# Kernel optimization log

Measured on AMD Instinct MI355X. Metric: run time of the kernel, lower is better.

The kernel has to match this reference:

```python
import jax, jax.numpy as jnp
import numpy as np

Y_SCALE = 1.0   # from init_kwargs
EPS = 1e-12     # matches torch F.normalize eps


def _l2_normalize(x):
    n = jnp.linalg.norm(x, axis=-1, keepdims=True)
    return x / jnp.maximum(n, EPS)


def _sequence_similarity(a, b):
    # a: [B, N, D], b: [B, M, D]
    a = _l2_normalize(a)
    b = _l2_normalize(b)
    cos_sims = jnp.einsum('bnd,bmd->bnm', a, b)  # [B, N, M]
    if cos_sims.shape[-1] > cos_sims.shape[-2]:
        max_sims = cos_sims.max(axis=-1)  # [B, N]
    else:
        max_sims = cos_sims.max(axis=-2)  # [B, M]
    return max_sims.mean(axis=-1)  # [B]


def setup_inputs() -> dict:
    key = jax.random.key(0)
    k1, k2, k3 = jax.random.split(key, 3)
    B, N, M, D = 16, 4096, 2048, 256
    x1 = jax.random.normal(k1, (B, N, D), dtype=jnp.float32)
    x2 = jax.random.normal(k2, (B, M, D), dtype=jnp.float32)
    y = jax.random.uniform(k3, (B,), dtype=jnp.float32)
    return {"x1": x1, "x2": x2, "y": y}


def reference(x1, x2, y):
    raw_sim_scores = _sequence_similarity(x1, x2)  # [B]
    losses = (raw_sim_scores - y) ** 2
    scales = jnp.where(y != 0.0, jnp.float32(Y_SCALE), jnp.float32(1.0))
    return (losses * scales).sum()
```

## Files before the change

### kernel.cpp

```cpp
#include <hip/hip_runtime.h>
#include <hip/hip_bf16.h>
#include <cstdint>
#include <cstddef>

#define BATCH 16
#define NROWS 4096
#define MROWS 2048
#define DDIM  256
#define NSPLIT 2
#define NCHUNKS 8

typedef __attribute__((ext_vector_type(8)))  int   i32x8;
typedef __attribute__((ext_vector_type(16))) float f32x16;

__global__ void __launch_bounds__(256) norm_cast(
    const float* __restrict__ x1, const float* __restrict__ x2,
    unsigned char* __restrict__ aout, unsigned char* __restrict__ bout) {
  const int wid  = threadIdx.x >> 6;
  const int lane = threadIdx.x & 63;
  const long long row = (long long)blockIdx.x * 4 + wid;
  const long long R1 = (long long)BATCH * NROWS;
  const long long R2 = (long long)BATCH * MROWS;
  if (row >= R1 + R2) return;
  const float* src; unsigned char* dst;
  if (row < R1) { src = x1 + row * DDIM; dst = aout + row * DDIM; }
  else { long long r2 = row - R1; src = x2 + r2 * DDIM; dst = bout + r2 * DDIM; }
  float4 v = ((const float4*)src)[lane];
  float ss = v.x*v.x + v.y*v.y + v.z*v.z + v.w*v.w;
  #pragma unroll
  for (int o = 32; o >= 1; o >>= 1) ss += __shfl_xor(ss, o, 64);
  float sc = 1.0f / fmaxf(sqrtf(ss), 1e-12f);
  int r = __builtin_amdgcn_cvt_pk_fp8_f32(v.x * sc, v.y * sc, 0, false);
  r = __builtin_amdgcn_cvt_pk_fp8_f32(v.z * sc, v.w * sc, r, true);
  ((unsigned int*)dst)[lane] = (unsigned int)r;
}

typedef __attribute__((address_space(1))) const void gas_t;
typedef __attribute__((address_space(3))) void las_t;
#define GLL16(g, l) __builtin_amdgcn_global_load_lds((gas_t*)(g), (las_t*)(l), 16, 0, 0)

#define LDSA(S) (lds + ((S) << 14))
#define LDSB(S) (lds + 65536 + ((S) << 14))

static __device__ __forceinline__ i32x8 frag8(const char* slot, int row, int lane) {
  const int rb = (lane >> 1) & 3;
  const int ks = lane >> 5;
  const char* base = slot + row * 64;
  uint4 u0 = *(const uint4*)(base + ((((ks << 1) | 0) ^ rb) << 4));
  uint4 u1 = *(const uint4*)(base + ((((ks << 1) | 1) ^ rb) << 4));
  i32x8 r;
  r[0] = u0.x; r[1] = u0.y; r[2] = u0.z; r[3] = u0.w;
  r[4] = u1.x; r[5] = u1.y; r[6] = u1.z; r[7] = u1.w;
  return r;
}

__global__ void __launch_bounds__(512, 1) maxsim_fp8(
    const unsigned char* __restrict__ A,
    const unsigned char* __restrict__ Bm,
    float* __restrict__ partials)
{
  __shared__ __align__(16) char lds[131072];

  const int t = threadIdx.x;
  const int lane = t & 63;
  const int w = t >> 6;
  const int wr = w >> 2;
  const int wc = w & 3;
  const int l31 = lane & 31;

  const int hw = blockIdx.x;
  const int logical = (hw & 7) * 32 + (hw >> 3);
  const int mt = logical & 7;
  const int grp = logical >> 3;
  const int sp = grp & 1;
  const int bb = grp >> 1;

  const int m0 = mt * 256;
  const int nbase = sp * (NROWS / NSPLIT);

  const unsigned char* Aba = A  + (size_t)bb * NROWS * DDIM;
  const unsigned char* Bba = Bm + ((size_t)bb * MROWS + m0) * DDIM;

  const int r0 = (w * 2 + 0) * 16 + (lane >> 2);
  const int r1 = (w * 2 + 1) * 16 + (lane >> 2);
  const int sph = (((lane & 3) ^ ((lane >> 3) & 3)) << 4);
  const unsigned char* sA0 = Aba + (size_t)r0 * DDIM + sph;
  const unsigned char* sA1 = Aba + (size_t)r1 * DDIM + sph;
  const unsigned char* sB0 = Bba + (size_t)r0 * DDIM + sph;
  const unsigned char* sB1 = Bba + (size_t)r1 * DDIM + sph;
  const int l0 = (w * 2 + 0) * 1024 + lane * 16;
  const int l1 = (w * 2 + 1) * 1024 + lane * 16;

  #define STAGE_A(SLOT, OFF) do { \
    GLL16(sA0 + (OFF), (SLOT) + l0); GLL16(sA1 + (OFF), (SLOT) + l1); } while (0)
  #define STAGE_B(SLOT, OFF) do { \
    GLL16(sB0 + (OFF), (SLOT) + l0); GLL16(sB1 + (OFF), (SLOT) + l1); } while (0)

  f32x16 acc[4][2] = {};
  const f32x16 z16 = {};
  i32x8 af[4];
  i32x8 bfAll[4][2];
  float cm[2] = {-INFINITY, -INFINITY};

  STAGE_A(LDSA(0), (size_t)nbase * DDIM + 0);
  STAGE_B(LDSB(0), 0);
  STAGE_B(LDSB(1), 64);
  STAGE_B(LDSB(2), 128);
  STAGE_B(LDSB(3), 192);
  STAGE_A(LDSA(1), (size_t)nbase * DDIM + 64);
  asm volatile("s_waitcnt vmcnt(2)" ::: "memory");
  asm volatile("s_barrier" ::: "memory");

  #pragma unroll
  for (int kt = 0; kt < 4; ++kt)
    #pragma unroll
    for (int nj = 0; nj < 2; ++nj)
      bfAll[kt][nj] = frag8(LDSB(kt), wc * 64 + nj * 32 + l31, lane);

  for (int nc = 0; nc < NCHUNKS; ++nc) {
    #pragma unroll
    for (int kt = 0; kt < 4; ++kt) {
      const char* sa = LDSA(kt);
      const int s2 = (kt + 2) & 3;
      const int nc2 = (kt < 2) ? nc : ((nc + 1) & (NCHUNKS - 1));
      const size_t offA2 = ((size_t)nbase + nc2 * 256) * DDIM + s2 * 64;

      #pragma unroll
      for (int mi = 0; mi < 4; ++mi)
        af[mi] = frag8(sa, wr * 128 + mi * 32 + l31, lane);
      STAGE_A(LDSA(s2), offA2);
      #pragma unroll
      for (int mi = 0; mi < 4; ++mi)
        #pragma unroll
        for (int nj = 0; nj < 2; ++nj)
          acc[mi][nj] = __builtin_amdgcn_mfma_scale_f32_32x32x64_f8f6f4(
              af[mi], bfAll[kt][nj], acc[mi][nj], 0, 0,
              0, 0x7F7F7F7F, 0, 0x7F7F7F7F);
      asm volatile("s_waitcnt vmcnt(2)" ::: "memory");
      asm volatile("s_barrier" ::: "memory");
    }
    #pragma unroll
    for (int nj = 0; nj < 2; ++nj) {
      float v = cm[nj];
      #pragma unroll
      for (int mi = 0; mi < 4; ++mi) {
        #pragma unroll
        for (int r = 0; r < 16; ++r) v = fmaxf(v, acc[mi][nj][r]);
        acc[mi][nj] = z16;
      }
      cm[nj] = v;
    }
  }

  asm volatile("s_waitcnt vmcnt(0)" ::: "memory");
  asm volatile("s_barrier" ::: "memory");
  #pragma unroll
  for (int nj = 0; nj < 2; ++nj)
    cm[nj] = fmaxf(cm[nj], __shfl_xor(cm[nj], 32, 64));
  float* cmax = (float*)lds;
  if (lane < 32) {
    cmax[wr * 256 + wc * 64 + l31]      = cm[0];
    cmax[wr * 256 + wc * 64 + 32 + l31] = cm[1];
  }
  __syncthreads();
  if (t < 256) {
    float v = fmaxf(cmax[t], cmax[256 + t]);
    partials[((size_t)sp * BATCH + bb) * MROWS + m0 + t] = v;
  }
}

__global__ void __launch_bounds__(256) batch_loss(
    const float* __restrict__ partials, const float* __restrict__ y,
    float* __restrict__ bloss) {
  __shared__ float red[4];
  const int b = blockIdx.x;
  const int t = threadIdx.x;
  const int lane = t & 63;
  const int w = t >> 6;
  float s = 0.0f;
  for (int m = t; m < MROWS; m += 256) {
    float v = partials[(size_t)b * MROWS + m];
    #pragma unroll
    for (int sp = 1; sp < NSPLIT; ++sp)
      v = fmaxf(v, partials[((size_t)sp * BATCH + b) * MROWS + m]);
    s += v;
  }
  #pragma unroll
  for (int o = 32; o >= 1; o >>= 1) s += __shfl_xor(s, o, 64);
  if (lane == 0) red[w] = s;
  __syncthreads();
  if (t == 0) {
    float sum = red[0] + red[1] + red[2] + red[3];
    float mean = sum / (float)MROWS;
    float yb = y[b];
    float d = mean - yb;
    bloss[b] = d * d;
  }
}

__global__ void __launch_bounds__(64) final_sum(
    const float* __restrict__ bloss, float* __restrict__ out) {
  const int t = threadIdx.x;
  float v = (t < BATCH) ? bloss[t] : 0.0f;
  #pragma unroll
  for (int o = 32; o >= 1; o >>= 1) v += __shfl_xor(v, o, 64);
  if (t == 0) out[0] = v;
}

extern "C" void kernel_launch(void* const* d_in, const int* in_sizes, int n_in,
                              void* d_out, int out_size, void* d_ws, size_t ws_size,
                              hipStream_t stream) {
  const float* x1 = (const float*)d_in[0];
  const float* x2 = (const float*)d_in[1];
  const float* y  = (const float*)d_in[2];
  float* out = (float*)d_out;

  unsigned char* aF8 = (unsigned char*)d_ws;
  unsigned char* bF8 = aF8 + (size_t)BATCH * NROWS * DDIM;
  float* partials = (float*)(bF8 + (size_t)BATCH * MROWS * DDIM);
  float* bloss = partials + (size_t)NSPLIT * BATCH * MROWS;

  const int totRows = BATCH * (NROWS + MROWS);
  norm_cast<<<(totRows + 3) / 4, 256, 0, stream>>>(x1, x2, aF8, bF8);
  maxsim_fp8<<<BATCH * 8 * NSPLIT, 512, 0, stream>>>(aF8, bF8, partials);
  batch_loss<<<BATCH, 256, 0, stream>>>(partials, y, bloss);
  final_sum<<<1, 64, 0, stream>>>(bloss, out);
}
```

Before: 54.82 us.

## Deepen A-tile prefetch ring to eight LDS slots and halve barrier count

```diff
diff --git a/kernel.cpp b/kernel.cpp
--- a/kernel.cpp
+++ b/kernel.cpp
@@ -39,8 +39,7 @@
 typedef __attribute__((address_space(3))) void las_t;
 #define GLL16(g, l) __builtin_amdgcn_global_load_lds((gas_t*)(g), (las_t*)(l), 16, 0, 0)
 
-#define LDSA(S) (lds + ((S) << 14))
-#define LDSB(S) (lds + 65536 + ((S) << 14))
+#define SLOT(S) (lds + ((S) << 14))
 
 static __device__ __forceinline__ i32x8 frag8(const char* slot, int row, int lane) {
   const int rb = (lane >> 1) & 3;
@@ -91,10 +90,12 @@
   const int l0 = (w * 2 + 0) * 1024 + lane * 16;
   const int l1 = (w * 2 + 1) * 1024 + lane * 16;
 
-  #define STAGE_A(SLOT, OFF) do { \
-    GLL16(sA0 + (OFF), (SLOT) + l0); GLL16(sA1 + (OFF), (SLOT) + l1); } while (0)
-  #define STAGE_B(SLOT, OFF) do { \
-    GLL16(sB0 + (OFF), (SLOT) + l0); GLL16(sB1 + (OFF), (SLOT) + l1); } while (0)
+  #define STAGE_A(SL, OFF) do { \
+    GLL16(sA0 + (OFF), (SL) + l0); GLL16(sA1 + (OFF), (SL) + l1); } while (0)
+  #define STAGE_B(SL, OFF) do { \
+    GLL16(sB0 + (OFF), (SL) + l0); GLL16(sB1 + (OFF), (SL) + l1); } while (0)
+
+  #define AOFF(G) (((size_t)nbase + (((G) >> 2) & 7) * 256) * DDIM + ((G) & 3) * 64)
 
   f32x16 acc[4][2] = {};
   const f32x16 z16 = {};
@@ -102,53 +103,78 @@
   i32x8 bfAll[4][2];
   float cm[2] = {-INFINITY, -INFINITY};
 
-  STAGE_A(LDSA(0), (size_t)nbase * DDIM + 0);
-  STAGE_B(LDSB(0), 0);
-  STAGE_B(LDSB(1), 64);
-  STAGE_B(LDSB(2), 128);
-  STAGE_B(LDSB(3), 192);
-  STAGE_A(LDSA(1), (size_t)nbase * DDIM + 64);
-  asm volatile("s_waitcnt vmcnt(2)" ::: "memory");
+  STAGE_A(SLOT(0), AOFF(0));
+  STAGE_B(SLOT(4), 0);
+  STAGE_B(SLOT(5), 64);
+  STAGE_B(SLOT(6), 128);
+  STAGE_B(SLOT(7), 192);
+  STAGE_A(SLOT(1), AOFF(1));
+  STAGE_A(SLOT(2), AOFF(2));
+  STAGE_A(SLOT(3), AOFF(3));
+  asm volatile("s_waitcnt vmcnt(0)" ::: "memory");
   asm volatile("s_barrier" ::: "memory");
 
   #pragma unroll
   for (int kt = 0; kt < 4; ++kt)
     #pragma unroll
     for (int nj = 0; nj < 2; ++nj)
-      bfAll[kt][nj] = frag8(LDSB(kt), wc * 64 + nj * 32 + l31, lane);
-
-  for (int nc = 0; nc < NCHUNKS; ++nc) {
+      bfAll[kt][nj] = frag8(SLOT(4 + kt), wc * 64 + nj * 32 + l31, lane);
+  asm volatile("s_waitcnt lgkmcnt(0)" ::: "memory");
+  asm volatile("s_barrier" ::: "memory");
+  STAGE_A(SLOT(4), AOFF(4));
+  STAGE_A(SLOT(5), AOFF(5));
+
+  for (int jj = 0; jj < 4; ++jj) {
     #pragma unroll
-    for (int kt = 0; kt < 4; ++kt) {
-      const char* sa = LDSA(kt);
-      const int s2 = (kt + 2) & 3;
-      const int nc2 = (kt < 2) ? nc : ((nc + 1) & (NCHUNKS - 1));
-      const size_t offA2 = ((size_t)nbase + nc2 * 256) * DDIM + s2 * 64;
-
-      #pragma unroll
-      for (int mi = 0; mi < 4; ++mi)
-        af[mi] = frag8(sa, wr * 128 + mi * 32 + l31, lane);
-      STAGE_A(LDSA(s2), offA2);
+    for (int p = 0; p < 4; ++p) {
+      const int J = jj * 4 + p;
+      const int sa0 = 2 * p;
+      const int sa1 = 2 * p + 1;
+      const int st0 = (2 * p + 6) & 7;
+      const int st1 = (2 * p + 7) & 7;
+      const int kt0 = (2 * p) & 3;
+      const int kt1 = (2 * p + 1) & 3;
+      const int g0 = (2 * J + 6) & 31;
+      const int g1 = (2 * J + 7) & 31;
+
+      #pragma unroll
+      for (int mi = 0; mi < 4; ++mi)
+        af[mi] = frag8(SLOT(sa0), wr * 128 + mi * 32 + l31, lane);
+      STAGE_A(SLOT(st0), AOFF(g0));
+      STAGE_A(SLOT(st1), AOFF(g1));
       #pragma unroll
       for (int mi = 0; mi < 4; ++mi)
         #pragma unroll
         for (int nj = 0; nj < 2; ++nj)
           acc[mi][nj] = __builtin_amdgcn_mfma_scale_f32_32x32x64_f8f6f4(
-              af[mi], bfAll[kt][nj], acc[mi][nj], 0, 0,
+              af[mi], bfAll[kt0][nj], acc[mi][nj], 0, 0,
               0, 0x7F7F7F7F, 0, 0x7F7F7F7F);
-      asm volatile("s_waitcnt vmcnt(2)" ::: "memory");
+      #pragma unroll
+      for (int mi = 0; mi < 4; ++mi)
+        af[mi] = frag8(SLOT(sa1), wr * 128 + mi * 32 + l31, lane);
+      #pragma unroll
+      for (int mi = 0; mi < 4; ++mi)
+        #pragma unroll
+        for (int nj = 0; nj < 2; ++nj)
+          acc[mi][nj] = __builtin_amdgcn_mfma_scale_f32_32x32x64_f8f6f4(
+              af[mi], bfAll[kt1][nj], acc[mi][nj], 0, 0,
+              0, 0x7F7F7F7F, 0, 0x7F7F7F7F);
+
+      if (p & 1) {
+        #pragma unroll
+        for (int nj = 0; nj < 2; ++nj) {
+          float v = cm[nj];
+          #pragma unroll
+          for (int mi = 0; mi < 4; ++mi) {
+            #pragma unroll
+            for (int r = 0; r < 16; ++r) v = fmaxf(v, acc[mi][nj][r]);
+            acc[mi][nj] = z16;
+          }
+          cm[nj] = v;
+        }
+      }
+      asm volatile("s_waitcnt vmcnt(8)" ::: "memory");
       asm volatile("s_barrier" ::: "memory");
-    }
-    #pragma unroll
-    for (int nj = 0; nj < 2; ++nj) {
-      float v = cm[nj];
-      #pragma unroll
-      for (int mi = 0; mi < 4; ++mi) {
-        #pragma unroll
-        for (int r = 0; r < 16; ++r) v = fmaxf(v, acc[mi][nj][r]);
-        acc[mi][nj] = z16;
-      }
-      cm[nj] = v;
     }
   }
 
```

Result: slower. 59.67 us (+8.9%).
